# Kernel tuning notes

Measured on AMD Instinct MI355X. Metric: run time of the kernel, lower is better.

## Reference

```python
import jax, jax.numpy as jnp
import numpy as np

B, C1, D1, C2, D2 = 128, 1152, 8, 10, 16
ROUTING_ITERS = 3


def squash(s, axis=-1, eps=1e-8):
    # squash(s) = (|s|^2 / (1+|s|^2)) * s / sqrt(|s|^2 + eps)
    sq = jnp.sum(s * s, axis=axis, keepdims=True)
    return (sq / (1.0 + sq)) * s / jnp.sqrt(sq + eps)


def setup_inputs() -> dict:
    key = jax.random.key(0)
    k1, k2, k3 = jax.random.split(key, 3)
    inputs = jax.random.normal(k1, (B, C1 * D1), dtype=jnp.float32)
    # W: (caps1, caps2, d2, d1), truncated normal stddev=0.1 (leading batch-1 dim dropped)
    W = jax.random.truncated_normal(k2, -2.0, 2.0, (C1, C2, D2, D1), dtype=jnp.float32) * 0.1
    # routing bias: (1, 1, caps2, d2)
    bias = jax.random.normal(k3, (1, 1, C2, D2), dtype=jnp.float32) * 0.1
    return {"inputs": inputs, "W": W, "bias": bias}


def reference(inputs, W, bias):
    b = inputs.shape[0]
    # PrimaryCaps: reshape to [B, C1, D1] then squash over the capsule dim (axis=-2 of
    # the original [B, C1, 1, D1, 1] tensor == D1 here)
    prim = squash(inputs.reshape(b, C1, D1), axis=-1)
    # DigitalCaps (fast): u_hat[b,i,j,:] = W[i,j] @ prim[b,i]  -> [B, C1, C2, D2]
    u_hat = jnp.einsum('cjdk,bck->bcjd', W, prim)
    u_stop = jax.lax.stop_gradient(u_hat)
    raw = jnp.zeros((b, C1, C2, 1), dtype=inputs.dtype)
    v = None
    for r in range(ROUTING_ITERS):
        u = u_hat if r == ROUTING_ITERS - 1 else u_stop
        c = jax.nn.softmax(raw, axis=2)                      # softmax over output caps
        s = jnp.sum(c * u, axis=1, keepdims=True) + bias     # [B, 1, C2, D2]
        v = squash(s, axis=-1)                               # squash over D2 (orig axis=-2)
        if r != ROUTING_ITERS - 1:
            # agreement: sum over D2 of u * v (v broadcasts over C1)
            raw = raw + jnp.sum(u * v, axis=-1, keepdims=True)
    # original returns [B, 1, C2, D2, 1]
    return v[..., None]
```

## Files before the change

kernel.cpp:

```cpp
#include <hip/hip_runtime.h>
#include <hip/hip_fp16.h>

#define BATCH 128
#define NC1   1152
#define ND1   8
#define NC2   10
#define ND2   16
#define SDIM  (NC2 * ND2)

#define CB 16
#define BB 32

#define NQ   6
#define QCAP (NC1 / NQ)
#define CPGP (QCAP / 32)

__device__ __forceinline__ unsigned pack_h2(float a, float b) {
    __half2 h = __floats2half2_rn(a, b);
    return *reinterpret_cast<unsigned*>(&h);
}
__device__ __forceinline__ float2 unpack_h2(unsigned v) {
    __half2 h = *reinterpret_cast<__half2*>(&v);
    return __half22float2(h);
}
__device__ __forceinline__ unsigned pmul_h2(unsigned a, unsigned b) {
    __half2 ha = *reinterpret_cast<__half2*>(&a);
    __half2 hb = *reinterpret_cast<__half2*>(&b);
    __half2 r = __hmul2(ha, hb);
    return *reinterpret_cast<unsigned*>(&r);
}
__device__ __forceinline__ unsigned padd_h2(unsigned a, unsigned b) {
    __half2 ha = *reinterpret_cast<__half2*>(&a);
    __half2 hb = *reinterpret_cast<__half2*>(&b);
    __half2 r = __hadd2(ha, hb);
    return *reinterpret_cast<unsigned*>(&r);
}

template<int CTRL>
__device__ __forceinline__ unsigned dpp_mov(unsigned v) {
    return (unsigned)__builtin_amdgcn_mov_dpp((int)v, CTRL, 0xF, 0xF, true);
}
__device__ __forceinline__ unsigned row_reduce_h2(unsigned t2) {
    t2 = padd_h2(t2, dpp_mov<0x128>(t2));
    t2 = padd_h2(t2, dpp_mov<0x124>(t2));
    t2 = padd_h2(t2, dpp_mov<0x122>(t2));
    t2 = padd_h2(t2, dpp_mov<0x121>(t2));
    return t2;
}

__global__ void caps_zero(float* __restrict__ s0) {
    s0[blockIdx.x * 256 + threadIdx.x] = 0.0f;
}

__global__ __launch_bounds__(256, 2) void caps_uhat(
    const float* __restrict__ x,
    const float* __restrict__ W,
    unsigned* __restrict__ u_ws,
    float* __restrict__ s0)
{
    const int cb  = blockIdx.x;
    const int bb  = blockIdx.y;
    const int tid = threadIdx.x;
    const int cl  = tid >> 4;
    const int d   = tid & 15;
    const int wl  = tid & 63;

    __shared__ float prim[BB][CB][ND1];

    for (int i = tid; i < BB * CB; i += 256) {
        const int b = i >> 4, c = i & 15;
        const float* xr = x + ((size_t)(bb * BB + b) * NC1 + (cb * CB + c)) * ND1;
        float4 a0 = *(const float4*)(xr);
        float4 a1 = *(const float4*)(xr + 4);
        float sq = a0.x*a0.x + a0.y*a0.y + a0.z*a0.z + a0.w*a0.w
                 + a1.x*a1.x + a1.y*a1.y + a1.z*a1.z + a1.w*a1.w;
        float g = (sq / (1.0f + sq)) * rsqrtf(sq + 1e-8f);
        prim[b][c][0] = a0.x * g; prim[b][c][1] = a0.y * g;
        prim[b][c][2] = a0.z * g; prim[b][c][3] = a0.w * g;
        prim[b][c][4] = a1.x * g; prim[b][c][5] = a1.y * g;
        prim[b][c][6] = a1.z * g; prim[b][c][7] = a1.w * g;
    }
    __syncthreads();

    const int c_glob = cb * CB + cl;
    unsigned wpk[NC2][4];
    #pragma unroll
    for (int j = 0; j < NC2; ++j) {
        const float* Wr = W + (((size_t)c_glob * NC2 + j) * ND2 + d) * ND1;
        float4 w0 = *(const float4*)(Wr);
        float4 w1 = *(const float4*)(Wr + 4);
        wpk[j][0] = pack_h2(w0.x, w0.y);
        wpk[j][1] = pack_h2(w0.z, w0.w);
        wpk[j][2] = pack_h2(w1.x, w1.y);
        wpk[j][3] = pack_h2(w1.z, w1.w);
    }

    for (int k = 0; k < BB; ++k) {
        const int b = (k + cb) & (BB - 1);
        const int bglob = bb * BB + b;
        float p[ND1];
        #pragma unroll
        for (int kk = 0; kk < ND1; ++kk) p[kk] = prim[b][cl][kk];

        unsigned* ur = u_ws + ((size_t)bglob * 5 * NC1 + c_glob) * 16 + d;
        #pragma unroll
        for (int jp = 0; jp < 5; ++jp) {
            float u0 = 0.f, u1 = 0.f;
            #pragma unroll
            for (int kp = 0; kp < 4; ++kp) {
                float2 fa = unpack_h2(wpk[2*jp  ][kp]);
                float2 fb = unpack_h2(wpk[2*jp+1][kp]);
                u0 += fa.x * p[2*kp] + fa.y * p[2*kp+1];
                u1 += fb.x * p[2*kp] + fb.y * p[2*kp+1];
            }
            unsigned pk = pack_h2(u0, u1);
            ur[(size_t)jp * (NC1 * 16)] = pk;
            pk = padd_h2(pk, (unsigned)__shfl_xor((int)pk, 16));
            pk = padd_h2(pk, (unsigned)__shfl_xor((int)pk, 32));
            if (wl < 16) {
                float2 f = unpack_h2(pk);
                atomicAdd(&s0[(size_t)bglob * SDIM + (2*jp)   * 16 + d], f.x);
                atomicAdd(&s0[(size_t)bglob * SDIM + (2*jp+1) * 16 + d], f.y);
            }
        }
    }
}

__global__ __launch_bounds__(512, 1) void caps_pass(
    const unsigned* __restrict__ u_ws,
    const float* __restrict__ s0,
    const float* __restrict__ spart_in,
    const float* __restrict__ bias,
    float* __restrict__ spart_out,
    int mode)
{
    const int bx   = blockIdx.x;
    const int b    = bx / NQ;
    const int q    = bx % NQ;
    const int tid  = threadIdx.x;
    const int grp  = tid >> 4;
    const int d    = tid & 15;
    const int wave = tid >> 6;

    __shared__ float vl[SDIM];
    __shared__ float sred[8][SDIM];

    const unsigned* ub = u_ws + (size_t)b * 5 * NC1 * 16 + d;
    const int c0 = q * QCAP + grp;
    unsigned uo[CPGP][5];
    #pragma unroll
    for (int i = 0; i < CPGP; ++i) {
        const int c = c0 + i * 32;
        #pragma unroll
        for (int jp = 0; jp < 5; ++jp)
            uo[i][jp] = ub[(size_t)jp * (NC1 * 16) + (size_t)c * 16];
    }

    if (tid < SDIM) {
        float bv = bias[tid];
        float s_a = 0.1f * s0[(size_t)b * SDIM + tid] + bv;
        float qa = s_a * s_a;
        qa += __shfl_xor(qa, 1); qa += __shfl_xor(qa, 2);
        qa += __shfl_xor(qa, 4); qa += __shfl_xor(qa, 8);
        float v = (qa / (1.0f + qa)) * rsqrtf(qa + 1e-8f) * s_a;
        if (mode == 1) {
            float s_b = bv;
            #pragma unroll
            for (int qq = 0; qq < NQ; ++qq)
                s_b += spart_in[((size_t)b * NQ + qq) * SDIM + tid];
            float qb = s_b * s_b;
            qb += __shfl_xor(qb, 1); qb += __shfl_xor(qb, 2);
            qb += __shfl_xor(qb, 4); qb += __shfl_xor(qb, 8);
            v += (qb / (1.0f + qb)) * rsqrtf(qb + 1e-8f) * s_b;
        }
        vl[tid] = v;
    }
    __syncthreads();

    unsigned vsf[5];
    #pragma unroll
    for (int jp = 0; jp < 5; ++jp)
        vsf[jp] = pack_h2(vl[(2*jp)*16 + d], vl[(2*jp+1)*16 + d]);

    float sp[NC2];
    #pragma unroll
    for (int j = 0; j < NC2; ++j) sp[j] = 0.0f;

    #pragma unroll
    for (int i = 0; i < CPGP; ++i) {
        float u[NC2], r[NC2];
        #pragma unroll
        for (int jp = 0; jp < 5; ++jp) {
            float2 f = unpack_h2(uo[i][jp]);
            u[2*jp] = f.x; u[2*jp+1] = f.y;
            unsigned t2 = row_reduce_h2(pmul_h2(uo[i][jp], vsf[jp]));
            float2 rr = unpack_h2(t2);
            r[2*jp] = rr.x; r[2*jp+1] = rr.y;
        }
        float ssum = 0.0f;
        #pragma unroll
        for (int j = 0; j < NC2; ++j) { r[j] = __expf(r[j]); ssum += r[j]; }
        float inv = 1.0f / ssum;
        #pragma unroll
        for (int j = 0; j < NC2; ++j) sp[j] += (r[j] * inv) * u[j];
    }

    #pragma unroll
    for (int j = 0; j < NC2; ++j) {
        sp[j] += __shfl_xor(sp[j], 16);
        sp[j] += __shfl_xor(sp[j], 32);
    }
    if ((tid & 63) < 16) {
        #pragma unroll
        for (int j = 0; j < NC2; ++j) sred[wave][j * 16 + d] = sp[j];
    }
    __syncthreads();
    if (tid < SDIM) {
        float acc = 0.0f;
        #pragma unroll
        for (int w = 0; w < 8; ++w) acc += sred[w][tid];
        spart_out[((size_t)b * NQ + q) * SDIM + tid] = acc;
    }
}

__global__ void caps_comb2(const float* __restrict__ spart,
                           const float* __restrict__ bias,
                           float* __restrict__ out) {
    const int b = blockIdx.x, tid = threadIdx.x;
    if (tid >= SDIM) return;
    float s = bias[tid];
    #pragma unroll
    for (int q = 0; q < NQ; ++q)
        s += spart[((size_t)b * NQ + q) * SDIM + tid];
    float sq = s * s;
    sq += __shfl_xor(sq, 1); sq += __shfl_xor(sq, 2);
    sq += __shfl_xor(sq, 4); sq += __shfl_xor(sq, 8);
    out[(size_t)b * SDIM + tid] = (sq / (1.0f + sq)) * rsqrtf(sq + 1e-8f) * s;
}

__global__ __launch_bounds__(1024) void caps_fused(
    const float* __restrict__ x, const float* __restrict__ W,
    const float* __restrict__ bias, float* __restrict__ out)
{
    const int b    = blockIdx.x;
    const int tid  = threadIdx.x;
    const int grp  = tid >> 4;
    const int d    = tid & 15;
    const int wave = tid >> 6;
    const int lane = tid & 63;

    __shared__ float prim[NC1][ND1];
    __shared__ float sred[16][SDIM];
    __shared__ float vbuf[SDIM];

    const float* xb = x + (size_t)b * (NC1 * ND1);
    for (int c = tid; c < NC1; c += 1024) {
        float4 a0 = *(const float4*)(xb + c * 8);
        float4 a1 = *(const float4*)(xb + c * 8 + 4);
        float sq = a0.x*a0.x + a0.y*a0.y + a0.z*a0.z + a0.w*a0.w
                 + a1.x*a1.x + a1.y*a1.y + a1.z*a1.z + a1.w*a1.w;
        float g = (sq / (1.0f + sq)) * rsqrtf(sq + 1e-8f);
        prim[c][0] = a0.x * g; prim[c][1] = a0.y * g;
        prim[c][2] = a0.z * g; prim[c][3] = a0.w * g;
        prim[c][4] = a1.x * g; prim[c][5] = a1.y * g;
        prim[c][6] = a1.z * g; prim[c][7] = a1.w * g;
    }
    __syncthreads();

    float vsum[NC2], sp[NC2];
    for (int pass = 0; pass < 3; ++pass) {
        #pragma unroll
        for (int j = 0; j < NC2; ++j) sp[j] = 0.0f;
        for (int c = grp; c < NC1; c += 64) {
            float p[8];
            #pragma unroll
            for (int k = 0; k < 8; ++k) p[k] = prim[c][k];
            const float* Wc = W + (size_t)c * (NC2 * ND2 * ND1) + d * ND1;
            float u[NC2];
            #pragma unroll
            for (int j = 0; j < NC2; ++j) {
                const float4 w0 = *(const float4*)(Wc + j * (ND2 * ND1));
                const float4 w1 = *(const float4*)(Wc + j * (ND2 * ND1) + 4);
                u[j] = w0.x*p[0] + w0.y*p[1] + w0.z*p[2] + w0.w*p[3]
                     + w1.x*p[4] + w1.y*p[5] + w1.z*p[6] + w1.w*p[7];
            }
            if (pass == 0) {
                #pragma unroll
                for (int j = 0; j < NC2; ++j) sp[j] += u[j];
            } else {
                float r[NC2];
                #pragma unroll
                for (int j = 0; j < NC2; ++j) {
                    float t = u[j] * vsum[j];
                    t += __shfl_xor(t, 1); t += __shfl_xor(t, 2);
                    t += __shfl_xor(t, 4); t += __shfl_xor(t, 8);
                    r[j] = t;
                }
                float m = r[0];
                #pragma unroll
                for (int j = 1; j < NC2; ++j) m = fmaxf(m, r[j]);
                float ssum = 0.0f;
                #pragma unroll
                for (int j = 0; j < NC2; ++j) { r[j] = __expf(r[j] - m); ssum += r[j]; }
                float inv = 1.0f / ssum;
                #pragma unroll
                for (int j = 0; j < NC2; ++j) sp[j] += (r[j] * inv) * u[j];
            }
        }
        #pragma unroll
        for (int j = 0; j < NC2; ++j) {
            sp[j] += __shfl_xor(sp[j], 16);
            sp[j] += __shfl_xor(sp[j], 32);
        }
        if (lane < 16) {
            #pragma unroll
            for (int j = 0; j < NC2; ++j) sred[wave][j * 16 + d] = sp[j];
        }
        __syncthreads();
        if (tid < SDIM) {
            float acc = 0.0f;
            #pragma unroll
            for (int w = 0; w < 16; ++w) acc += sred[w][tid];
            float s = bias[tid] + (pass == 0 ? 0.1f * acc : acc);
            float sq = s * s;
            sq += __shfl_xor(sq, 1); sq += __shfl_xor(sq, 2);
            sq += __shfl_xor(sq, 4); sq += __shfl_xor(sq, 8);
            float vv = (sq / (1.0f + sq)) * rsqrtf(sq + 1e-8f) * s;
            if (pass == 2) out[(size_t)b * SDIM + tid] = vv;
            else           vbuf[tid] = vv;
        }
        __syncthreads();
        if (pass < 2) {
            #pragma unroll
            for (int j = 0; j < NC2; ++j) {
                float vv = vbuf[j * 16 + d];
                vsum[j] = (pass == 0) ? vv : (vsum[j] + vv);
            }
        }
        __syncthreads();
    }
}

extern "C" void kernel_launch(void* const* d_in, const int* in_sizes, int n_in,
                              void* d_out, int out_size, void* d_ws, size_t ws_size,
                              hipStream_t stream) {
    const float* x    = (const float*)d_in[0];
    const float* W    = (const float*)d_in[1];
    const float* bias = (const float*)d_in[2];
    float* out = (float*)d_out;

    const size_t u_bytes  = (size_t)BATCH * 5 * NC1 * 16 * 4;
    const size_t s0_bytes = (size_t)BATCH * SDIM * 4;
    const size_t sp_bytes = (size_t)BATCH * NQ * SDIM * 4;
    const size_t need = u_bytes + s0_bytes + 2 * sp_bytes;

    if (ws_size >= need) {
        unsigned* u_ws  = (unsigned*)d_ws;
        float*    s0    = (float*)((char*)d_ws + u_bytes);
        float*    sp1   = (float*)((char*)d_ws + u_bytes + s0_bytes);
        float*    sp2   = (float*)((char*)d_ws + u_bytes + s0_bytes + sp_bytes);

        caps_zero <<<80, 256, 0, stream>>>(s0);
        caps_uhat <<<dim3(NC1 / CB, BATCH / BB), 256, 0, stream>>>(x, W, u_ws, s0);
        caps_pass <<<BATCH * NQ, 512, 0, stream>>>(u_ws, s0, sp1, bias, sp1, 0);
        caps_pass <<<BATCH * NQ, 512, 0, stream>>>(u_ws, s0, sp1, bias, sp2, 1);
        caps_comb2<<<BATCH, 192, 0, stream>>>(sp2, bias, out);
    } else {
        caps_fused<<<BATCH, 1024, 0, stream>>>(x, W, bias, out);
    }
}
```

Before: 72.10 us.

## Fuse routing passes into one cooperative kernel with grid syncs

```diff
diff --git a/kernel.cpp b/kernel.cpp
--- a/kernel.cpp
+++ b/kernel.cpp
@@ -1,5 +1,8 @@
 #include <hip/hip_runtime.h>
 #include <hip/hip_fp16.h>
+#include <hip/hip_cooperative_groups.h>
+
+namespace cg = cooperative_groups;
 
 #define BATCH 128
 #define NC1   1152
@@ -7,13 +10,11 @@
 #define NC2   10
 #define ND2   16
 #define SDIM  (NC2 * ND2)
+#define HALFC (NC1 / 2)
+#define CPH   18
 
 #define CB 16
 #define BB 32
-
-#define NQ   6
-#define QCAP (NC1 / NQ)
-#define CPGP (QCAP / 32)
 
 __device__ __forceinline__ unsigned pack_h2(float a, float b) {
     __half2 h = __floats2half2_rn(a, b);
@@ -126,17 +127,17 @@
     }
 }
 
-__global__ __launch_bounds__(512, 1) void caps_pass(
+__global__ __launch_bounds__(512, 1) void caps_route2(
     const unsigned* __restrict__ u_ws,
     const float* __restrict__ s0,
-    const float* __restrict__ spart_in,
     const float* __restrict__ bias,
-    float* __restrict__ spart_out,
-    int mode)
+    float* __restrict__ spart1,
+    float* __restrict__ spart2,
+    float* __restrict__ out)
 {
-    const int bx   = blockIdx.x;
-    const int b    = bx / NQ;
-    const int q    = bx % NQ;
+    const int blk  = blockIdx.x;
+    const int b    = blk >> 1;
+    const int h    = blk & 1;
     const int tid  = threadIdx.x;
     const int grp  = tid >> 4;
     const int d    = tid & 15;
@@ -145,16 +146,73 @@
     __shared__ float vl[SDIM];
     __shared__ float sred[8][SDIM];
 
+    cg::grid_group grid = cg::this_grid();
+
     const unsigned* ub = u_ws + (size_t)b * 5 * NC1 * 16 + d;
-    const int c0 = q * QCAP + grp;
-    unsigned uo[CPGP][5];
-    #pragma unroll
-    for (int i = 0; i < CPGP; ++i) {
+    const int c0 = h * HALFC + grp;
+    unsigned uo[CPH][5];
+    #pragma unroll
+    for (int i = 0; i < CPH; ++i) {
         const int c = c0 + i * 32;
         #pragma unroll
         for (int jp = 0; jp < 5; ++jp)
             uo[i][jp] = ub[(size_t)jp * (NC1 * 16) + (size_t)c * 16];
     }
+
+    if (tid < SDIM) {
+        float s_a = 0.1f * s0[(size_t)b * SDIM + tid] + bias[tid];
+        float qa = s_a * s_a;
+        qa += __shfl_xor(qa, 1); qa += __shfl_xor(qa, 2);
+        qa += __shfl_xor(qa, 4); qa += __shfl_xor(qa, 8);
+        vl[tid] = (qa / (1.0f + qa)) * rsqrtf(qa + 1e-8f) * s_a;
+    }
+    __syncthreads();
+
+    unsigned vsf[5];
+    #pragma unroll
+    for (int jp = 0; jp < 5; ++jp)
+        vsf[jp] = pack_h2(vl[(2*jp)*16 + d], vl[(2*jp+1)*16 + d]);
+
+    float sp[NC2];
+
+    #pragma unroll
+    for (int j = 0; j < NC2; ++j) sp[j] = 0.0f;
+    #pragma unroll
+    for (int i = 0; i < CPH; ++i) {
+        float u[NC2], r[NC2];
+        #pragma unroll
+        for (int jp = 0; jp < 5; ++jp) {
+            float2 f = unpack_h2(uo[i][jp]);
+            u[2*jp] = f.x; u[2*jp+1] = f.y;
+            unsigned t2 = row_reduce_h2(pmul_h2(uo[i][jp], vsf[jp]));
+            float2 rr = unpack_h2(t2);
+            r[2*jp] = rr.x; r[2*jp+1] = rr.y;
+        }
+        float ssum = 0.0f;
+        #pragma unroll
+        for (int j = 0; j < NC2; ++j) { r[j] = __expf(r[j]); ssum += r[j]; }
+        float inv = 1.0f / ssum;
+        #pragma unroll
+        for (int j = 0; j < NC2; ++j) sp[j] += (r[j] * inv) * u[j];
+    }
+    #pragma unroll
+    for (int j = 0; j < NC2; ++j) {
+        sp[j] += __shfl_xor(sp[j], 16);
+        sp[j] += __shfl_xor(sp[j], 32);
+    }
+    if ((tid & 63) < 16) {
+        #pragma unroll
+        for (int j = 0; j < NC2; ++j) sred[wave][j * 16 + d] = sp[j];
+    }
+    __syncthreads();
+    if (tid < SDIM) {
+        float acc = 0.0f;
+        #pragma unroll
+        for (int w = 0; w < 8; ++w) acc += sred[w][tid];
+        spart1[(size_t)(b * 2 + h) * SDIM + tid] = acc;
+    }
+
+    grid.sync();
 
     if (tid < SDIM) {
         float bv = bias[tid];
@@ -163,31 +221,24 @@
         qa += __shfl_xor(qa, 1); qa += __shfl_xor(qa, 2);
         qa += __shfl_xor(qa, 4); qa += __shfl_xor(qa, 8);
         float v = (qa / (1.0f + qa)) * rsqrtf(qa + 1e-8f) * s_a;
-        if (mode == 1) {
-            float s_b = bv;
-            #pragma unroll
-            for (int qq = 0; qq < NQ; ++qq)
-                s_b += spart_in[((size_t)b * NQ + qq) * SDIM + tid];
-            float qb = s_b * s_b;
-            qb += __shfl_xor(qb, 1); qb += __shfl_xor(qb, 2);
-            qb += __shfl_xor(qb, 4); qb += __shfl_xor(qb, 8);
-            v += (qb / (1.0f + qb)) * rsqrtf(qb + 1e-8f) * s_b;
-        }
+        float s_b = spart1[(size_t)(b * 2 + 0) * SDIM + tid]
+                  + spart1[(size_t)(b * 2 + 1) * SDIM + tid] + bv;
+        float qb = s_b * s_b;
+        qb += __shfl_xor(qb, 1); qb += __shfl_xor(qb, 2);
+        qb += __shfl_xor(qb, 4); qb += __shfl_xor(qb, 8);
+        v += (qb / (1.0f + qb)) * rsqrtf(qb + 1e-8f) * s_b;
         vl[tid] = v;
     }
     __syncthreads();
 
-    unsigned vsf[5];
     #pragma unroll
     for (int jp = 0; jp < 5; ++jp)
         vsf[jp] = pack_h2(vl[(2*jp)*16 + d], vl[(2*jp+1)*16 + d]);
 
-    float sp[NC2];
     #pragma unroll
     for (int j = 0; j < NC2; ++j) sp[j] = 0.0f;
-
-    #pragma unroll
-    for (int i = 0; i < CPGP; ++i) {
+    #pragma unroll
+    for (int i = 0; i < CPH; ++i) {
         float u[NC2], r[NC2];
         #pragma unroll
         for (int jp = 0; jp < 5; ++jp) {
@@ -204,7 +255,6 @@
         #pragma unroll
         for (int j = 0; j < NC2; ++j) sp[j] += (r[j] * inv) * u[j];
     }
-
     #pragma unroll
     for (int j = 0; j < NC2; ++j) {
         sp[j] += __shfl_xor(sp[j], 16);
@@ -219,23 +269,19 @@
         float acc = 0.0f;
         #pragma unroll
         for (int w = 0; w < 8; ++w) acc += sred[w][tid];
-        spart_out[((size_t)b * NQ + q) * SDIM + tid] = acc;
-    }
-}
-
-__global__ void caps_comb2(const float* __restrict__ spart,
-                           const float* __restrict__ bias,
-                           float* __restrict__ out) {
-    const int b = blockIdx.x, tid = threadIdx.x;
-    if (tid >= SDIM) return;
-    float s = bias[tid];
-    #pragma unroll
-    for (int q = 0; q < NQ; ++q)
-        s += spart[((size_t)b * NQ + q) * SDIM + tid];
-    float sq = s * s;
-    sq += __shfl_xor(sq, 1); sq += __shfl_xor(sq, 2);
-    sq += __shfl_xor(sq, 4); sq += __shfl_xor(sq, 8);
-    out[(size_t)b * SDIM + tid] = (sq / (1.0f + sq)) * rsqrtf(sq + 1e-8f) * s;
+        spart2[(size_t)(b * 2 + h) * SDIM + tid] = acc;
+    }
+
+    grid.sync();
+
+    if (h == 0 && tid < SDIM) {
+        float s = spart2[(size_t)(b * 2 + 0) * SDIM + tid]
+                + spart2[(size_t)(b * 2 + 1) * SDIM + tid] + bias[tid];
+        float sq = s * s;
+        sq += __shfl_xor(sq, 1); sq += __shfl_xor(sq, 2);
+        sq += __shfl_xor(sq, 4); sq += __shfl_xor(sq, 8);
+        out[(size_t)b * SDIM + tid] = (sq / (1.0f + sq)) * rsqrtf(sq + 1e-8f) * s;
+    }
 }
 
 __global__ __launch_bounds__(1024) void caps_fused(
@@ -351,7 +397,7 @@
 
     const size_t u_bytes  = (size_t)BATCH * 5 * NC1 * 16 * 4;
     const size_t s0_bytes = (size_t)BATCH * SDIM * 4;
-    const size_t sp_bytes = (size_t)BATCH * NQ * SDIM * 4;
+    const size_t sp_bytes = (size_t)BATCH * 2 * SDIM * 4;
     const size_t need = u_bytes + s0_bytes + 2 * sp_bytes;
 
     if (ws_size >= need) {
@@ -362,9 +408,10 @@
 
         caps_zero <<<80, 256, 0, stream>>>(s0);
         caps_uhat <<<dim3(NC1 / CB, BATCH / BB), 256, 0, stream>>>(x, W, u_ws, s0);
-        caps_pass <<<BATCH * NQ, 512, 0, stream>>>(u_ws, s0, sp1, bias, sp1, 0);
-        caps_pass <<<BATCH * NQ, 512, 0, stream>>>(u_ws, s0, sp1, bias, sp2, 1);
-        caps_comb2<<<BATCH, 192, 0, stream>>>(sp2, bias, out);
+        void* args[] = {(void*)&u_ws, (void*)&s0, (void*)&bias,
+                        (void*)&sp1, (void*)&sp2, (void*)&out};
+        hipLaunchCooperativeKernel((const void*)caps_route2,
+                                   dim3(BATCH * 2), dim3(512), args, 0, stream);
     } else {
         caps_fused<<<BATCH, 1024, 0, stream>>>(x, W, bias, out);
     }
```

After: 139.8 us. +93.9%, slower.
